# Kernel optimization log

Hardware: AMD Instinct MI355X
Metric: run time of the kernel (lower is better)

Reference implementation:

```python
import jax, jax.numpy as jnp
import numpy as np

B, T, V, E, H, N = 8, 128, 32000, 128, 256, 20
SHARPEN = 5.0
EPS = 1e-8  # torch cosine_similarity eps


def setup_inputs() -> dict:
    key = jax.random.key(0)
    ks = jax.random.split(key, 8)
    g = lambda k, shape, scale: (jax.random.normal(k, shape, dtype=jnp.float32) * scale)
    return {
        "x_ids": jax.random.randint(ks[0], (B, T), 0, V),
        "emb": g(ks[1], (V, E), 0.02),                 # nn.Embedding weight
        "W_i": g(ks[2], (H, E), E ** -0.5),            # rnn_i weight (no bias)
        "W_h": g(ks[3], (H, H), H ** -0.5),            # rnn_h weight
        "W_fc": g(ks[4], (V, 2 * H), (2 * H) ** -0.5), # fc -> vocab (softmaxed)
        "W_ops": g(ks[5], (3, 2 * H), (2 * H) ** -0.5),
        "W_choose": g(ks[6], (2, 2 * H), (2 * H) ** -0.5),
        "sharp": jnp.array([SHARPEN], dtype=jnp.float32),
    }


def _l2norm(x, eps=1e-12):
    # F.normalize(x, dim=-1)
    n = jnp.linalg.norm(x, axis=-1, keepdims=True)
    return x / jnp.maximum(n, eps)


def reference(x_ids, emb, W_i, W_h, W_fc, W_ops, W_choose, sharp):
    x = emb[x_ids]                                   # [B,T,E]
    # pre-normalize vocab rows for cosine-sim readout (clamped like torch)
    emb_cn = emb / jnp.maximum(jnp.linalg.norm(emb, axis=1, keepdims=True), EPS)
    sh = sharp[0]

    stack0 = jnp.full((B, N, E), 0.001, dtype=x.dtype)      # zero_offset + 0.001
    ptr0 = jnp.zeros((B, N), x.dtype).at[:, 0].set(1.0)     # pointer at slot 0
    h0 = jnp.zeros((B, H), x.dtype)

    def step(carry, xi):
        h, stack, ptr = carry
        ri = _l2norm(xi) @ W_i.T                     # rnn_i(normalize(x_t))
        h = jnp.tanh(ri + h @ W_h.T)
        hm = 1.0 - jax.nn.relu(h)
        hmod = jnp.concatenate([hm, hm], axis=1)     # [B,2H]
        # GumbelSoftmax(temp=1, hard=False) -> deterministic softmax (no noise)
        ops = jax.nn.softmax(hmod @ W_ops.T, axis=1)  # [B,3]
        push, pop, nop = ops[:, 0], ops[:, 1], ops[:, 2]
        # --- differentiable stack push/pop/nop ---
        pop_val = jnp.einsum('bn,bne->be', ptr, stack)      # soft read at pointer
        p_push = jnp.roll(ptr, 1, axis=1)
        p_pop = jnp.roll(ptr, -1, axis=1)
        new_ptr = push[:, None] * p_push + pop[:, None] * p_pop + nop[:, None] * ptr
        new_ptr = jnp.clip(new_ptr, EPS) ** sh              # sharpen
        new_ptr = new_ptr / jnp.sum(new_ptr, axis=1, keepdims=True)
        w = (push[:, None] * p_push)[:, :, None]            # write weight [B,N,1]
        new_stack = stack * (1.0 - w) + w * xi[:, None, :]
        # --- readout ---
        semantic = jax.nn.softmax(hmod @ W_fc.T, axis=1)    # [B,V]
        pv_n = pop_val / jnp.maximum(
            jnp.linalg.norm(pop_val, axis=1, keepdims=True), EPS)
        syntactic = pv_n @ emb_cn.T                          # cosine sim [B,V]
        choice = jax.nn.softmax(hmod @ W_choose.T, axis=1)   # [B,2]
        out = choice[:, 0:1] * semantic + choice[:, 1:2] * syntactic
        return (h, new_stack, new_ptr), out

    _, outs = jax.lax.scan(step, (h0, stack0, ptr0), jnp.swapaxes(x, 0, 1))
    return jnp.swapaxes(outs, 0, 1)  # [B,T,V]
```

## Files before the change

### kernel.cpp

```cpp
#include <hip/hip_runtime.h>
#include <hip/hip_bf16.h>
#include <stdint.h>

#define T_ 128
#define B_ 8
#define V_ 32000
#define E_ 128
#define H_ 256
#define N_ 20
#define M_ 1024
#define PIT 264
#define PIT2 136
#define NCH2 1000

typedef __attribute__((ext_vector_type(8))) short short8;
typedef __attribute__((ext_vector_type(4))) float f32x4;
typedef unsigned short ushort;

static __device__ __forceinline__ ushort f2bf_u(float f) {
  __hip_bfloat16 h = __float2bfloat16(f);
  return *reinterpret_cast<ushort*>(&h);
}

__global__ void whb_k(const float* __restrict__ Wh, uint4* __restrict__ whb4) {
  int idx = blockIdx.x*256 + threadIdx.x;
  int k8 = idx >> 8, i = idx & 255;
  const float* s = Wh + i*H_ + k8*8;
  uint4 o;
  o.x = (uint32_t)f2bf_u(s[0]) | ((uint32_t)f2bf_u(s[1]) << 16);
  o.y = (uint32_t)f2bf_u(s[2]) | ((uint32_t)f2bf_u(s[3]) << 16);
  o.z = (uint32_t)f2bf_u(s[4]) | ((uint32_t)f2bf_u(s[5]) << 16);
  o.w = (uint32_t)f2bf_u(s[6]) | ((uint32_t)f2bf_u(s[7]) << 16);
  whb4[idx] = o;
}

__global__ void wit_k(const float* __restrict__ Wi, float* __restrict__ WiT) {
  int idx = blockIdx.x*256 + threadIdx.x;
  if (idx < H_*E_) {
    int i = idx >> 7, e = idx & (E_-1);
    WiT[e*H_ + i] = Wi[idx];
  }
}

__global__ void embn_k(const float* __restrict__ emb, ushort* __restrict__ embnb) {
  int v = blockIdx.x, l = threadIdx.x;
  float e0 = emb[v*E_ + l];
  float e1 = emb[v*E_ + 64 + l];
  float ss = e0*e0 + e1*e1;
  #pragma unroll
  for (int off = 32; off >= 1; off >>= 1) ss += __shfl_xor(ss, off);
  float inv = 1.f / fmaxf(sqrtf(ss), 1e-8f);
  embnb[v*E_ + l]      = f2bf_u(e0*inv);
  embnb[v*E_ + 64 + l] = f2bf_u(e1*inv);
}

__global__ void foldfc_k(const float* __restrict__ Wfc, ushort* __restrict__ Wfcb) {
  int idx = blockIdx.x*256 + threadIdx.x;
  int n = idx >> 8, k = idx & 255;
  Wfcb[idx] = f2bf_u(Wfc[n*2*H_ + k] + Wfc[n*2*H_ + H_ + k]);
}

__global__ __launch_bounds__(256) void ri_k(const int* __restrict__ x_ids,
    const float* __restrict__ emb, const float* __restrict__ WiT,
    float* __restrict__ RI)
{
  __shared__ float xn[E_];
  __shared__ float red[2];
  int r = blockIdx.x, tid = threadIdx.x;
  int id = x_ids[r];
  float v = 0.f;
  if (tid < E_) v = emb[id*E_ + tid];
  float ss = v*v;
  if (tid < E_) {
    #pragma unroll
    for (int off = 32; off >= 1; off >>= 1) ss += __shfl_xor(ss, off);
    if ((tid & 63) == 0) red[tid >> 6] = ss;
  }
  __syncthreads();
  float inv = 1.f / fmaxf(sqrtf(red[0] + red[1]), 1e-12f);
  if (tid < E_) xn[tid] = v*inv;
  __syncthreads();
  float s = 0.f;
  for (int e = 0; e < E_; ++e) s += xn[e]*WiT[e*H_ + tid];
  RI[r*H_ + tid] = s;
}

__global__ __launch_bounds__(1024) void chain_k(
    const uint4* __restrict__ whb4, const float* __restrict__ RI,
    float* __restrict__ HMf, ushort* __restrict__ HMb)
{
  __shared__ uint4 wlds[32*256];
  __shared__ __align__(16) float hbuf[2][H_];
  __shared__ float hred[3][H_];
  const int b = blockIdx.x, tid = threadIdx.x;
  const int q = tid >> 8, i = tid & 255;

  for (int m = tid; m < 32*256; m += 1024) wlds[m] = whb4[m];
  if (q == 0) hbuf[0][i] = 0.f;
  __syncthreads();
  float ri_c = (q == 0) ? RI[(size_t)b*T_*H_ + i] : 0.f;

  for (int t = 0; t < T_; ++t) {
    const int r = b*T_ + t;
    float ri_n = 0.f;
    if (q == 0 && t+1 < T_) ri_n = RI[(size_t)(r+1)*H_ + i];
    const float4* h4 = reinterpret_cast<const float4*>(hbuf[t & 1]);
    float p0 = 0.f, p1 = 0.f, p2 = 0.f, p3 = 0.f;
    #pragma unroll
    for (int j = 0; j < 8; ++j) {
      uint4 w = wlds[(q*8 + j)*256 + i];
      float4 ha = h4[q*16 + 2*j];
      float4 hb = h4[q*16 + 2*j + 1];
      p0 += __uint_as_float(w.x << 16)*ha.x + __uint_as_float(w.x & 0xffff0000u)*ha.y;
      p1 += __uint_as_float(w.y << 16)*ha.z + __uint_as_float(w.y & 0xffff0000u)*ha.w;
      p2 += __uint_as_float(w.z << 16)*hb.x + __uint_as_float(w.z & 0xffff0000u)*hb.y;
      p3 += __uint_as_float(w.w << 16)*hb.z + __uint_as_float(w.w & 0xffff0000u)*hb.w;
    }
    float p = (p0 + p1) + (p2 + p3);
    if (q) hred[q-1][i] = p;
    __syncthreads();
    if (q == 0) {
      float s = ri_c + p + hred[0][i] + hred[1][i] + hred[2][i];
      float hn = tanhf(s);
      hbuf[(t+1) & 1][i] = hn;
      float hm = 1.f - fmaxf(hn, 0.f);
      HMf[(size_t)r*H_ + i] = hm;
      HMb[(size_t)r*H_ + i] = f2bf_u(hm);
    }
    ri_c = ri_n;
    __syncthreads();
  }
}

__global__ void dots_k(const float* __restrict__ HMf,
    const float* __restrict__ W_ops, const float* __restrict__ W_ch,
    float* __restrict__ OPS, float* __restrict__ CH)
{
  int r = blockIdx.x, l = threadIdx.x;
  float4 hm4 = reinterpret_cast<const float4*>(HMf + (size_t)r*H_)[l];
  float d[5];
  #pragma unroll
  for (int k = 0; k < 3; ++k) {
    float w0 = W_ops[k*2*H_ + 4*l+0] + W_ops[k*2*H_ + H_ + 4*l+0];
    float w1 = W_ops[k*2*H_ + 4*l+1] + W_ops[k*2*H_ + H_ + 4*l+1];
    float w2 = W_ops[k*2*H_ + 4*l+2] + W_ops[k*2*H_ + H_ + 4*l+2];
    float w3 = W_ops[k*2*H_ + 4*l+3] + W_ops[k*2*H_ + H_ + 4*l+3];
    d[k] = hm4.x*w0 + hm4.y*w1 + hm4.z*w2 + hm4.w*w3;
  }
  #pragma unroll
  for (int k = 0; k < 2; ++k) {
    float w0 = W_ch[k*2*H_ + 4*l+0] + W_ch[k*2*H_ + H_ + 4*l+0];
    float w1 = W_ch[k*2*H_ + 4*l+1] + W_ch[k*2*H_ + H_ + 4*l+1];
    float w2 = W_ch[k*2*H_ + 4*l+2] + W_ch[k*2*H_ + H_ + 4*l+2];
    float w3 = W_ch[k*2*H_ + 4*l+3] + W_ch[k*2*H_ + H_ + 4*l+3];
    d[3+k] = hm4.x*w0 + hm4.y*w1 + hm4.z*w2 + hm4.w*w3;
  }
  #pragma unroll
  for (int off = 32; off >= 1; off >>= 1)
    #pragma unroll
    for (int k = 0; k < 5; ++k) d[k] += __shfl_xor(d[k], off);
  if (l == 0) {
    float mx = fmaxf(d[0], fmaxf(d[1], d[2]));
    float e0 = expf(d[0]-mx), e1 = expf(d[1]-mx), e2 = expf(d[2]-mx);
    float oi = 1.f/(e0+e1+e2);
    OPS[r*4+0] = e0*oi; OPS[r*4+1] = e1*oi; OPS[r*4+2] = e2*oi;
    float cm = fmaxf(d[3], d[4]);
    float f0 = expf(d[3]-cm), f1 = expf(d[4]-cm);
    float ci = 1.f/(f0+f1);
    CH[r*2] = f0*ci; CH[r*2+1] = f1*ci;
  }
}

__global__ __launch_bounds__(64) void ptrw_k(const float* __restrict__ OPS,
    const float* __restrict__ sharp, float2* __restrict__ PTRW)
{
  __shared__ float ops_s[T_*4];
  const int b = blockIdx.x, l = threadIdx.x;
  for (int m = l; m < T_*4; m += 64) ops_s[m] = OPS[(size_t)b*T_*4 + m];
  const float sh = sharp[0];
  float ptr = (l == 0) ? 1.f : 0.f;
  const int lp = (l + N_ - 1) % N_;
  const int ln = (l + 1) % N_;
  for (int t = 0; t < T_; ++t) {
    float push = ops_s[t*4+0], pop = ops_s[t*4+1], nop = ops_s[t*4+2];
    float pp = __shfl(ptr, lp);
    float po = __shfl(ptr, ln);
    float w = push*pp;
    float raw = w + pop*po + nop*ptr;
    float np = 0.f;
    if (l < N_) np = exp2f(sh * log2f(fmaxf(raw, 1e-8f)));
    float ssum = np;
    #pragma unroll
    for (int off = 1; off < 32; off <<= 1) ssum += __shfl_xor(ssum, off);
    if (l < N_) {
      PTRW[(size_t)(b*T_ + t)*N_ + l] = make_float2(ptr, w);
      ptr = np / ssum;
    }
  }
}

__global__ __launch_bounds__(128) void pv_k(const int* __restrict__ x_ids,
    const float* __restrict__ emb, const float2* __restrict__ PTRW,
    float* __restrict__ PV)
{
  __shared__ float2 pw_s[T_*N_];
  __shared__ int ids_s[T_];
  const int b = blockIdx.x, e = threadIdx.x;
  for (int m = e; m < T_*N_; m += 128) pw_s[m] = PTRW[(size_t)b*T_*N_ + m];
  if (e < T_) ids_s[e] = x_ids[b*T_ + e];
  __syncthreads();
  float stck[N_];
  #pragma unroll
  for (int n = 0; n < N_; ++n) stck[n] = 0.001f;
  float xi_c = emb[(size_t)ids_s[0]*E_ + e];
  for (int t = 0; t < T_; ++t) {
    float xi_n = (t+1 < T_) ? emb[(size_t)ids_s[t+1]*E_ + e] : 0.f;
    float pv = 0.f;
    #pragma unroll
    for (int n = 0; n < N_; ++n) {
      float2 pw = pw_s[t*N_ + n];
      pv += pw.x * stck[n];
      stck[n] += pw.y * (xi_c - stck[n]);
    }
    PV[(size_t)(b*T_ + t)*E_ + e] = pv;
    xi_c = xi_n;
  }
}

__global__ void pvn_k(const float* __restrict__ PV, ushort* __restrict__ PVNb) {
  int r = blockIdx.x, l = threadIdx.x;
  float a = PV[(size_t)r*E_ + l];
  float c = PV[(size_t)r*E_ + 64 + l];
  float ss = a*a + c*c;
  #pragma unroll
  for (int off = 32; off >= 1; off >>= 1) ss += __shfl_xor(ss, off);
  float inv = 1.f / fmaxf(sqrtf(ss), 1e-8f);
  PVNb[(size_t)r*E_ + l]      = f2bf_u(a*inv);
  PVNb[(size_t)r*E_ + 64 + l] = f2bf_u(c*inv);
}

__global__ __launch_bounds__(256) void stats2_k(const ushort* __restrict__ HMb,
    const ushort* __restrict__ Wfcb, float* __restrict__ SS)
{
  __shared__ __align__(16) ushort As[64*PIT];
  __shared__ __align__(16) ushort Bs[64*PIT];
  const int tid = threadIdx.x;
  const int Rb = blockIdx.y*64, Cb = blockIdx.x*64;
  const uint4* srcA = (const uint4*)(HMb  + (size_t)Rb*H_);
  const uint4* srcB = (const uint4*)(Wfcb + (size_t)Cb*H_);
  #pragma unroll
  for (int it = 0; it < 8; ++it) {
    int idx = it*256 + tid, row = idx >> 5, c = idx & 31;
    *(uint4*)&As[row*PIT + c*8] = srcA[row*32 + c];
    *(uint4*)&Bs[row*PIT + c*8] = srcB[row*32 + c];
  }
  __syncthreads();

  const int wave = tid >> 6, lane = tid & 63;
  const int wr = wave >> 1, wc = wave & 1;
  const int lr = lane & 15, g = lane >> 4;
  f32x4 acc[2][2] = {};
  const ushort* Ab = &As[(wr*32 + lr)*PIT + g*8];
  const ushort* Bb = &Bs[(wc*32 + lr)*PIT + g*8];
  #pragma unroll
  for (int ks = 0; ks < 8; ++ks) {
    short8 a0 = *(const short8*)(Ab + ks*32);
    short8 a1 = *(const short8*)(Ab + 16*PIT + ks*32);
    short8 b0 = *(const short8*)(Bb + ks*32);
    short8 b1 = *(const short8*)(Bb + 16*PIT + ks*32);
    acc[0][0] = __builtin_amdgcn_mfma_f32_16x16x32_bf16(a0, b0, acc[0][0], 0, 0, 0);
    acc[0][1] = __builtin_amdgcn_mfma_f32_16x16x32_bf16(a0, b1, acc[0][1], 0, 0, 0);
    acc[1][0] = __builtin_amdgcn_mfma_f32_16x16x32_bf16(a1, b0, acc[1][0], 0, 0, 0);
    acc[1][1] = __builtin_amdgcn_mfma_f32_16x16x32_bf16(a1, b1, acc[1][1], 0, 0, 0);
  }
  const int chunk = blockIdx.x*2 + wc;
  #pragma unroll
  for (int mi = 0; mi < 2; ++mi)
    #pragma unroll
    for (int r = 0; r < 4; ++r) {
      float s = expf(acc[mi][0][r]) + expf(acc[mi][1][r]);
      #pragma unroll
      for (int off = 1; off < 16; off <<= 1) s += __shfl_xor(s, off);
      if (lr == 0) SS[(size_t)(Rb + wr*32 + mi*16 + g*4 + r)*NCH2 + chunk] = s;
    }
}

__global__ void reduce2_k(const float* __restrict__ SS, float* __restrict__ MS) {
  int row = blockIdx.x, l = threadIdx.x;
  float s = 0.f;
  for (int c = l; c < NCH2; c += 64) s += SS[(size_t)row*NCH2 + c];
  #pragma unroll
  for (int off = 32; off >= 1; off >>= 1) s += __shfl_xor(s, off);
  if (l == 0) MS[row] = 1.f/s;
}

__global__ __launch_bounds__(256) void final2_k(const ushort* __restrict__ HMb,
    const ushort* __restrict__ Wfcb, const ushort* __restrict__ PVNb,
    const ushort* __restrict__ embnb, const float* __restrict__ MS,
    const float* __restrict__ CH, float* __restrict__ out)
{
  __shared__ __align__(16) ushort As[64*PIT];
  __shared__ __align__(16) ushort Bs[64*PIT];
  const int tid = threadIdx.x;
  const int Rb = blockIdx.y*64, Cb = blockIdx.x*64;
  const int wave = tid >> 6, lane = tid & 63;
  const int wr = wave >> 1, wc = wave & 1;
  const int lr = lane & 15, g = lane >> 4;

  {
    const uint4* srcA = (const uint4*)(HMb  + (size_t)Rb*H_);
    const uint4* srcB = (const uint4*)(Wfcb + (size_t)Cb*H_);
    #pragma unroll
    for (int it = 0; it < 8; ++it) {
      int idx = it*256 + tid, row = idx >> 5, c = idx & 31;
      *(uint4*)&As[row*PIT + c*8] = srcA[row*32 + c];
      *(uint4*)&Bs[row*PIT + c*8] = srcB[row*32 + c];
    }
  }
  __syncthreads();
  f32x4 accL[2][2] = {};
  {
    const ushort* Ab = &As[(wr*32 + lr)*PIT + g*8];
    const ushort* Bb = &Bs[(wc*32 + lr)*PIT + g*8];
    #pragma unroll
    for (int ks = 0; ks < 8; ++ks) {
      short8 a0 = *(const short8*)(Ab + ks*32);
      short8 a1 = *(const short8*)(Ab + 16*PIT + ks*32);
      short8 b0 = *(const short8*)(Bb + ks*32);
      short8 b1 = *(const short8*)(Bb + 16*PIT + ks*32);
      accL[0][0] = __builtin_amdgcn_mfma_f32_16x16x32_bf16(a0, b0, accL[0][0], 0, 0, 0);
      accL[0][1] = __builtin_amdgcn_mfma_f32_16x16x32_bf16(a0, b1, accL[0][1], 0, 0, 0);
      accL[1][0] = __builtin_amdgcn_mfma_f32_16x16x32_bf16(a1, b0, accL[1][0], 0, 0, 0);
      accL[1][1] = __builtin_amdgcn_mfma_f32_16x16x32_bf16(a1, b1, accL[1][1], 0, 0, 0);
    }
  }
  __syncthreads();

  {
    const uint4* srcA = (const uint4*)(PVNb  + (size_t)Rb*E_);
    const uint4* srcB = (const uint4*)(embnb + (size_t)Cb*E_);
    #pragma unroll
    for (int it = 0; it < 4; ++it) {
      int idx = it*256 + tid, row = idx >> 4, c = idx & 15;
      *(uint4*)&As[row*PIT2 + c*8] = srcA[row*16 + c];
      *(uint4*)&Bs[row*PIT2 + c*8] = srcB[row*16 + c];
    }
  }
  __syncthreads();
  f32x4 accS[2][2] = {};
  {
    const ushort* Ab = &As[(wr*32 + lr)*PIT2 + g*8];
    const ushort* Bb = &Bs[(wc*32 + lr)*PIT2 + g*8];
    #pragma unroll
    for (int ks = 0; ks < 4; ++ks) {
      short8 a0 = *(const short8*)(Ab + ks*32);
      short8 a1 = *(const short8*)(Ab + 16*PIT2 + ks*32);
      short8 b0 = *(const short8*)(Bb + ks*32);
      short8 b1 = *(const short8*)(Bb + 16*PIT2 + ks*32);
      accS[0][0] = __builtin_amdgcn_mfma_f32_16x16x32_bf16(a0, b0, accS[0][0], 0, 0, 0);
      accS[0][1] = __builtin_amdgcn_mfma_f32_16x16x32_bf16(a0, b1, accS[0][1], 0, 0, 0);
      accS[1][0] = __builtin_amdgcn_mfma_f32_16x16x32_bf16(a1, b0, accS[1][0], 0, 0, 0);
      accS[1][1] = __builtin_amdgcn_mfma_f32_16x16x32_bf16(a1, b1, accS[1][1], 0, 0, 0);
    }
  }

  #pragma unroll
  for (int mi = 0; mi < 2; ++mi)
    #pragma unroll
    for (int r = 0; r < 4; ++r) {
      int row = Rb + wr*32 + mi*16 + g*4 + r;
      float Si = MS[row];
      float c0 = CH[row*2], c1 = CH[row*2+1];
      float v0 = c0*expf(accL[mi][0][r])*Si + c1*accS[mi][0][r];
      float v1 = c0*expf(accL[mi][1][r])*Si + c1*accS[mi][1][r];
      size_t base = (size_t)row*V_ + Cb + wc*32 + lr;
      out[base]      = v0;
      out[base + 16] = v1;
    }
}

extern "C" void kernel_launch(void* const* d_in, const int* in_sizes, int n_in,
                              void* d_out, int out_size, void* d_ws, size_t ws_size,
                              hipStream_t stream) {
  const int*   x_ids = (const int*)d_in[0];
  const float* emb   = (const float*)d_in[1];
  const float* W_i   = (const float*)d_in[2];
  const float* W_h   = (const float*)d_in[3];
  const float* W_fc  = (const float*)d_in[4];
  const float* W_ops = (const float*)d_in[5];
  const float* W_ch  = (const float*)d_in[6];
  const float* sharp = (const float*)d_in[7];
  float* out = (float*)d_out;

  float* ws    = (float*)d_ws;
  uint4*  whb4 = (uint4*)ws;
  float*  WiT  = ws + 65536;
  float*  RI   = WiT + 32768;
  float*  CH   = RI + 262144;
  float*  MS   = CH + 2048;
  float*  SS   = MS + 1024;
  float*  HMf  = SS + 1024000;
  float*  OPS  = HMf + 262144;
  float*  PV   = OPS + 4096;
  float2* PTRW = (float2*)(PV + 131072);
  float*  fend = PV + 131072 + 40960;
  ushort* HMb   = (ushort*)fend;
  ushort* PVNb  = HMb + 262144;
  ushort* Wfcb  = PVNb + 131072;
  ushort* embnb = Wfcb + 8192000;

  whb_k  <<<32, 256, 0, stream>>>(W_h, whb4);
  wit_k  <<<(H_*E_ + 255)/256, 256, 0, stream>>>(W_i, WiT);
  embn_k <<<V_, 64, 0, stream>>>(emb, embnb);
  foldfc_k<<<V_*H_/256, 256, 0, stream>>>(W_fc, Wfcb);
  ri_k   <<<M_, 256, 0, stream>>>(x_ids, emb, WiT, RI);
  chain_k<<<B_, 1024, 0, stream>>>(whb4, RI, HMf, HMb);
  dots_k <<<M_, 64, 0, stream>>>(HMf, W_ops, W_ch, OPS, CH);
  ptrw_k <<<B_, 64, 0, stream>>>(OPS, sharp, PTRW);
  pv_k   <<<B_, 128, 0, stream>>>(x_ids, emb, PTRW, PV);
  pvn_k  <<<M_, 64, 0, stream>>>(PV, PVNb);
  stats2_k<<<dim3(V_/64, M_/64), 256, 0, stream>>>(HMb, Wfcb, SS);
  reduce2_k<<<M_, 64, 0, stream>>>(SS, MS);
  final2_k<<<dim3(V_/64, M_/64), 256, 0, stream>>>(HMb, Wfcb, PVNb, embnb, MS, CH, out);
}
```

Before: 437.3 us.

## Fold pointer/stack chain into stats GEMM kernel and use 128-row tiles

Removes the separate ops-dot, pointer-recurrence and stack-readout kernels. Their work now runs in an extra grid row of the softmax-statistics GEMM kernel, one block per batch, so the serial stack chain can overlap the GEMM and several launches and intermediate global buffers go away. The stats and final GEMM kernels also move from 64x64 tiles with 256 threads to 128x64 tiles with 512 threads, so each W_fc tile is reused across more rows. The risks are that the chain blocks sit in the last grid row and may be dispatched late, cutting the overlap, and that the larger shared-memory footprint lowers occupancy.

```diff
diff --git a/kernel.cpp b/kernel.cpp
--- a/kernel.cpp
+++ b/kernel.cpp
@@ -132,101 +132,6 @@
   }
 }
 
-__global__ void dots_k(const float* __restrict__ HMf,
-    const float* __restrict__ W_ops, const float* __restrict__ W_ch,
-    float* __restrict__ OPS, float* __restrict__ CH)
-{
-  int r = blockIdx.x, l = threadIdx.x;
-  float4 hm4 = reinterpret_cast<const float4*>(HMf + (size_t)r*H_)[l];
-  float d[5];
-  #pragma unroll
-  for (int k = 0; k < 3; ++k) {
-    float w0 = W_ops[k*2*H_ + 4*l+0] + W_ops[k*2*H_ + H_ + 4*l+0];
-    float w1 = W_ops[k*2*H_ + 4*l+1] + W_ops[k*2*H_ + H_ + 4*l+1];
-    float w2 = W_ops[k*2*H_ + 4*l+2] + W_ops[k*2*H_ + H_ + 4*l+2];
-    float w3 = W_ops[k*2*H_ + 4*l+3] + W_ops[k*2*H_ + H_ + 4*l+3];
-    d[k] = hm4.x*w0 + hm4.y*w1 + hm4.z*w2 + hm4.w*w3;
-  }
-  #pragma unroll
-  for (int k = 0; k < 2; ++k) {
-    float w0 = W_ch[k*2*H_ + 4*l+0] + W_ch[k*2*H_ + H_ + 4*l+0];
-    float w1 = W_ch[k*2*H_ + 4*l+1] + W_ch[k*2*H_ + H_ + 4*l+1];
-    float w2 = W_ch[k*2*H_ + 4*l+2] + W_ch[k*2*H_ + H_ + 4*l+2];
-    float w3 = W_ch[k*2*H_ + 4*l+3] + W_ch[k*2*H_ + H_ + 4*l+3];
-    d[3+k] = hm4.x*w0 + hm4.y*w1 + hm4.z*w2 + hm4.w*w3;
-  }
-  #pragma unroll
-  for (int off = 32; off >= 1; off >>= 1)
-    #pragma unroll
-    for (int k = 0; k < 5; ++k) d[k] += __shfl_xor(d[k], off);
-  if (l == 0) {
-    float mx = fmaxf(d[0], fmaxf(d[1], d[2]));
-    float e0 = expf(d[0]-mx), e1 = expf(d[1]-mx), e2 = expf(d[2]-mx);
-    float oi = 1.f/(e0+e1+e2);
-    OPS[r*4+0] = e0*oi; OPS[r*4+1] = e1*oi; OPS[r*4+2] = e2*oi;
-    float cm = fmaxf(d[3], d[4]);
-    float f0 = expf(d[3]-cm), f1 = expf(d[4]-cm);
-    float ci = 1.f/(f0+f1);
-    CH[r*2] = f0*ci; CH[r*2+1] = f1*ci;
-  }
-}
-
-__global__ __launch_bounds__(64) void ptrw_k(const float* __restrict__ OPS,
-    const float* __restrict__ sharp, float2* __restrict__ PTRW)
-{
-  __shared__ float ops_s[T_*4];
-  const int b = blockIdx.x, l = threadIdx.x;
-  for (int m = l; m < T_*4; m += 64) ops_s[m] = OPS[(size_t)b*T_*4 + m];
-  const float sh = sharp[0];
-  float ptr = (l == 0) ? 1.f : 0.f;
-  const int lp = (l + N_ - 1) % N_;
-  const int ln = (l + 1) % N_;
-  for (int t = 0; t < T_; ++t) {
-    float push = ops_s[t*4+0], pop = ops_s[t*4+1], nop = ops_s[t*4+2];
-    float pp = __shfl(ptr, lp);
-    float po = __shfl(ptr, ln);
-    float w = push*pp;
-    float raw = w + pop*po + nop*ptr;
-    float np = 0.f;
-    if (l < N_) np = exp2f(sh * log2f(fmaxf(raw, 1e-8f)));
-    float ssum = np;
-    #pragma unroll
-    for (int off = 1; off < 32; off <<= 1) ssum += __shfl_xor(ssum, off);
-    if (l < N_) {
-      PTRW[(size_t)(b*T_ + t)*N_ + l] = make_float2(ptr, w);
-      ptr = np / ssum;
-    }
-  }
-}
-
-__global__ __launch_bounds__(128) void pv_k(const int* __restrict__ x_ids,
-    const float* __restrict__ emb, const float2* __restrict__ PTRW,
-    float* __restrict__ PV)
-{
-  __shared__ float2 pw_s[T_*N_];
-  __shared__ int ids_s[T_];
-  const int b = blockIdx.x, e = threadIdx.x;
-  for (int m = e; m < T_*N_; m += 128) pw_s[m] = PTRW[(size_t)b*T_*N_ + m];
-  if (e < T_) ids_s[e] = x_ids[b*T_ + e];
-  __syncthreads();
-  float stck[N_];
-  #pragma unroll
-  for (int n = 0; n < N_; ++n) stck[n] = 0.001f;
-  float xi_c = emb[(size_t)ids_s[0]*E_ + e];
-  for (int t = 0; t < T_; ++t) {
-    float xi_n = (t+1 < T_) ? emb[(size_t)ids_s[t+1]*E_ + e] : 0.f;
-    float pv = 0.f;
-    #pragma unroll
-    for (int n = 0; n < N_; ++n) {
-      float2 pw = pw_s[t*N_ + n];
-      pv += pw.x * stck[n];
-      stck[n] += pw.y * (xi_c - stck[n]);
-    }
-    PV[(size_t)(b*T_ + t)*E_ + e] = pv;
-    xi_c = xi_n;
-  }
-}
-
 __global__ void pvn_k(const float* __restrict__ PV, ushort* __restrict__ PVNb) {
   int r = blockIdx.x, l = threadIdx.x;
   float a = PV[(size_t)r*E_ + l];
@@ -239,23 +144,121 @@
   PVNb[(size_t)r*E_ + 64 + l] = f2bf_u(c*inv);
 }
 
-__global__ __launch_bounds__(256) void stats2_k(const ushort* __restrict__ HMb,
-    const ushort* __restrict__ Wfcb, float* __restrict__ SS)
+__global__ __launch_bounds__(512) void stats3_k(const ushort* __restrict__ HMb,
+    const ushort* __restrict__ Wfcb, const float* __restrict__ HMf,
+    const float* __restrict__ W_ops, const float* __restrict__ W_ch,
+    const float* __restrict__ sharp, const int* __restrict__ x_ids,
+    const float* __restrict__ emb,
+    float* __restrict__ SS, float* __restrict__ CH, float* __restrict__ PV)
 {
-  __shared__ __align__(16) ushort As[64*PIT];
+  __shared__ __align__(16) ushort As[128*PIT];
   __shared__ __align__(16) ushort Bs[64*PIT];
+  __shared__ float ops_l[T_*4];
+  __shared__ float2 pw_l[T_*N_];
+  __shared__ int ids_l[T_];
   const int tid = threadIdx.x;
-  const int Rb = blockIdx.y*64, Cb = blockIdx.x*64;
-  const uint4* srcA = (const uint4*)(HMb  + (size_t)Rb*H_);
-  const uint4* srcB = (const uint4*)(Wfcb + (size_t)Cb*H_);
-  #pragma unroll
-  for (int it = 0; it < 8; ++it) {
-    int idx = it*256 + tid, row = idx >> 5, c = idx & 31;
-    *(uint4*)&As[row*PIT + c*8] = srcA[row*32 + c];
-    *(uint4*)&Bs[row*PIT + c*8] = srcB[row*32 + c];
-  }
-  __syncthreads();
-
+
+  if (blockIdx.y == 8) {
+    if (blockIdx.x >= B_) return;
+    const int b = blockIdx.x;
+    const int w = tid >> 6, l = tid & 63;
+    float wo[5][4];
+    #pragma unroll
+    for (int k = 0; k < 3; ++k)
+      #pragma unroll
+      for (int j = 0; j < 4; ++j)
+        wo[k][j] = W_ops[k*2*H_ + 4*l + j] + W_ops[k*2*H_ + H_ + 4*l + j];
+    #pragma unroll
+    for (int k = 0; k < 2; ++k)
+      #pragma unroll
+      for (int j = 0; j < 4; ++j)
+        wo[3+k][j] = W_ch[k*2*H_ + 4*l + j] + W_ch[k*2*H_ + H_ + 4*l + j];
+    if (tid < T_) ids_l[tid] = x_ids[b*T_ + tid];
+    for (int rl = w*16; rl < w*16 + 16; ++rl) {
+      int R = b*T_ + rl;
+      float4 hm4 = reinterpret_cast<const float4*>(HMf + (size_t)R*H_)[l];
+      float d0 = hm4.x*wo[0][0] + hm4.y*wo[0][1] + hm4.z*wo[0][2] + hm4.w*wo[0][3];
+      float d1 = hm4.x*wo[1][0] + hm4.y*wo[1][1] + hm4.z*wo[1][2] + hm4.w*wo[1][3];
+      float d2 = hm4.x*wo[2][0] + hm4.y*wo[2][1] + hm4.z*wo[2][2] + hm4.w*wo[2][3];
+      float d3 = hm4.x*wo[3][0] + hm4.y*wo[3][1] + hm4.z*wo[3][2] + hm4.w*wo[3][3];
+      float d4 = hm4.x*wo[4][0] + hm4.y*wo[4][1] + hm4.z*wo[4][2] + hm4.w*wo[4][3];
+      #pragma unroll
+      for (int off = 32; off >= 1; off >>= 1) {
+        d0 += __shfl_xor(d0, off); d1 += __shfl_xor(d1, off); d2 += __shfl_xor(d2, off);
+        d3 += __shfl_xor(d3, off); d4 += __shfl_xor(d4, off);
+      }
+      if (l == 0) {
+        float mx = fmaxf(d0, fmaxf(d1, d2));
+        float e0 = expf(d0-mx), e1 = expf(d1-mx), e2 = expf(d2-mx);
+        float oi = 1.f/(e0+e1+e2);
+        ops_l[rl*4+0] = e0*oi; ops_l[rl*4+1] = e1*oi; ops_l[rl*4+2] = e2*oi;
+        float cm = fmaxf(d3, d4);
+        float f0 = expf(d3-cm), f1 = expf(d4-cm);
+        float ci = 1.f/(f0+f1);
+        CH[R*2] = f0*ci; CH[R*2+1] = f1*ci;
+      }
+    }
+    __syncthreads();
+    if (tid < 64) {
+      const float sh = sharp[0];
+      float ptr = (tid == 0) ? 1.f : 0.f;
+      const int lp = (tid + N_ - 1) % N_, ln = (tid + 1) % N_;
+      for (int t = 0; t < T_; ++t) {
+        float push = ops_l[t*4+0], pop = ops_l[t*4+1], nop = ops_l[t*4+2];
+        float pp = __shfl(ptr, lp);
+        float po = __shfl(ptr, ln);
+        float wgt = push*pp;
+        float raw = wgt + pop*po + nop*ptr;
+        float np = 0.f;
+        if (tid < N_) np = exp2f(sh * log2f(fmaxf(raw, 1e-8f)));
+        float ssum = np;
+        #pragma unroll
+        for (int off = 1; off < 32; off <<= 1) ssum += __shfl_xor(ssum, off);
+        if (tid < N_) {
+          pw_l[t*N_ + tid] = make_float2(ptr, wgt);
+          ptr = np / ssum;
+        }
+      }
+    }
+    __syncthreads();
+    if (tid < E_) {
+      const int e = tid;
+      float stck[N_];
+      #pragma unroll
+      for (int n = 0; n < N_; ++n) stck[n] = 0.001f;
+      float xi_c = emb[(size_t)ids_l[0]*E_ + e];
+      for (int t = 0; t < T_; ++t) {
+        float xi_n = (t+1 < T_) ? emb[(size_t)ids_l[t+1]*E_ + e] : 0.f;
+        float pv = 0.f;
+        #pragma unroll
+        for (int n = 0; n < N_; ++n) {
+          float2 pw = pw_l[t*N_ + n];
+          pv += pw.x * stck[n];
+          stck[n] += pw.y * (xi_c - stck[n]);
+        }
+        PV[(size_t)(b*T_ + t)*E_ + e] = pv;
+        xi_c = xi_n;
+      }
+    }
+    return;
+  }
+
+  const int Rb = blockIdx.y*128, Cb = blockIdx.x*64;
+  {
+    const uint4* srcA = (const uint4*)(HMb  + (size_t)Rb*H_);
+    const uint4* srcB = (const uint4*)(Wfcb + (size_t)Cb*H_);
+    #pragma unroll
+    for (int it = 0; it < 8; ++it) {
+      int idx = it*512 + tid, row = idx >> 5, c = idx & 31;
+      *(uint4*)&As[row*PIT + c*8] = srcA[row*32 + c];
+    }
+    #pragma unroll
+    for (int it = 0; it < 4; ++it) {
+      int idx = it*512 + tid, row = idx >> 5, c = idx & 31;
+      *(uint4*)&Bs[row*PIT + c*8] = srcB[row*32 + c];
+    }
+  }
+  __syncthreads();
   const int wave = tid >> 6, lane = tid & 63;
   const int wr = wave >> 1, wc = wave & 1;
   const int lr = lane & 15, g = lane >> 4;
@@ -294,15 +297,15 @@
   if (l == 0) MS[row] = 1.f/s;
 }
 
-__global__ __launch_bounds__(256) void final2_k(const ushort* __restrict__ HMb,
+__global__ __launch_bounds__(512) void final3_k(const ushort* __restrict__ HMb,
     const ushort* __restrict__ Wfcb, const ushort* __restrict__ PVNb,
     const ushort* __restrict__ embnb, const float* __restrict__ MS,
     const float* __restrict__ CH, float* __restrict__ out)
 {
-  __shared__ __align__(16) ushort As[64*PIT];
+  __shared__ __align__(16) ushort As[128*PIT];
   __shared__ __align__(16) ushort Bs[64*PIT];
   const int tid = threadIdx.x;
-  const int Rb = blockIdx.y*64, Cb = blockIdx.x*64;
+  const int Rb = blockIdx.y*128, Cb = blockIdx.x*64;
   const int wave = tid >> 6, lane = tid & 63;
   const int wr = wave >> 1, wc = wave & 1;
   const int lr = lane & 15, g = lane >> 4;
@@ -312,8 +315,12 @@
     const uint4* srcB = (const uint4*)(Wfcb + (size_t)Cb*H_);
     #pragma unroll
     for (int it = 0; it < 8; ++it) {
-      int idx = it*256 + tid, row = idx >> 5, c = idx & 31;
+      int idx = it*512 + tid, row = idx >> 5, c = idx & 31;
       *(uint4*)&As[row*PIT + c*8] = srcA[row*32 + c];
+    }
+    #pragma unroll
+    for (int it = 0; it < 4; ++it) {
+      int idx = it*512 + tid, row = idx >> 5, c = idx & 31;
       *(uint4*)&Bs[row*PIT + c*8] = srcB[row*32 + c];
     }
   }
@@ -335,14 +342,17 @@
     }
   }
   __syncthreads();
-
   {
     const uint4* srcA = (const uint4*)(PVNb  + (size_t)Rb*E_);
     const uint4* srcB = (const uint4*)(embnb + (size_t)Cb*E_);
     #pragma unroll
     for (int it = 0; it < 4; ++it) {
-      int idx = it*256 + tid, row = idx >> 4, c = idx & 15;
+      int idx = it*512 + tid, row = idx >> 4, c = idx & 15;
       *(uint4*)&As[row*PIT2 + c*8] = srcA[row*16 + c];
+    }
+    #pragma unroll
+    for (int it = 0; it < 2; ++it) {
+      int idx = it*512 + tid, row = idx >> 4, c = idx & 15;
       *(uint4*)&Bs[row*PIT2 + c*8] = srcB[row*16 + c];
     }
   }
@@ -400,10 +410,8 @@
   float*  MS   = CH + 2048;
   float*  SS   = MS + 1024;
   float*  HMf  = SS + 1024000;
-  float*  OPS  = HMf + 262144;
-  float*  PV   = OPS + 4096;
-  float2* PTRW = (float2*)(PV + 131072);
-  float*  fend = PV + 131072 + 40960;
+  float*  PV   = HMf + 262144;
+  float*  fend = PV + 131072;
   ushort* HMb   = (ushort*)fend;
   ushort* PVNb  = HMb + 262144;
   ushort* Wfcb  = PVNb + 131072;
@@ -415,11 +423,9 @@
   foldfc_k<<<V_*H_/256, 256, 0, stream>>>(W_fc, Wfcb);
   ri_k   <<<M_, 256, 0, stream>>>(x_ids, emb, WiT, RI);
   chain_k<<<B_, 1024, 0, stream>>>(whb4, RI, HMf, HMb);
-  dots_k <<<M_, 64, 0, stream>>>(HMf, W_ops, W_ch, OPS, CH);
-  ptrw_k <<<B_, 64, 0, stream>>>(OPS, sharp, PTRW);
-  pv_k   <<<B_, 128, 0, stream>>>(x_ids, emb, PTRW, PV);
+  stats3_k<<<dim3(V_/64, 9), 512, 0, stream>>>(HMb, Wfcb, HMf, W_ops, W_ch, sharp,
+                                               x_ids, emb, SS, CH, PV);
   pvn_k  <<<M_, 64, 0, stream>>>(PV, PVNb);
-  stats2_k<<<dim3(V_/64, M_/64), 256, 0, stream>>>(HMb, Wfcb, SS);
   reduce2_k<<<M_, 64, 0, stream>>>(SS, MS);
-  final2_k<<<dim3(V_/64, M_/64), 256, 0, stream>>>(HMb, Wfcb, PVNb, embnb, MS, CH, out);
-}
+  final3_k<<<dim3(V_/64, M_/128), 512, 0, stream>>>(HMb, Wfcb, PVNb, embnb, MS, CH, out);
+}
```

New measurement: 443.0 us. Within noise of the previous version (+1.3%).
